# Kernel tuning notes

Hardware: AMD Instinct MI355X
Metric: run time of the kernel (lower is better)

## Reference

```python
import jax, jax.numpy as jnp
import numpy as np

N_HEAD = 8
LN_EPS = 1e-5


def _ln(x, g, b):
    m = jnp.mean(x, axis=-1, keepdims=True)
    v = jnp.mean((x - m) ** 2, axis=-1, keepdims=True)
    return (x - m) * jax.lax.rsqrt(v + LN_EPS) * g + b


def setup_inputs() -> dict:
    B, S, IN, D, F, OUT, L = 4, 2048, 3, 512, 2048, 20, 6
    key = jax.random.key(0)
    ks = jax.random.split(key, 22)
    sc = 0.02
    return {
        'src': jax.random.normal(ks[0], (B, S, IN), jnp.float32),
        'W_in': jax.random.normal(ks[1], (IN, D), jnp.float32) * sc,
        'b_in': jnp.zeros((D,), jnp.float32),
        'Wq': jax.random.normal(ks[2], (L, D, D), jnp.float32) * sc,
        'bq': jnp.zeros((L, D), jnp.float32),
        'Wk': jax.random.normal(ks[3], (L, D, D), jnp.float32) * sc,
        'bk': jnp.zeros((L, D), jnp.float32),
        'Wv': jax.random.normal(ks[4], (L, D, D), jnp.float32) * sc,
        'bv': jnp.zeros((L, D), jnp.float32),
        'Wo': jax.random.normal(ks[5], (L, D, D), jnp.float32) * sc,
        'bo': jnp.zeros((L, D), jnp.float32),
        'ln1_g': jnp.ones((L, D), jnp.float32),
        'ln1_b': jnp.zeros((L, D), jnp.float32),
        'W1': jax.random.normal(ks[6], (L, D, F), jnp.float32) * sc,
        'b1': jnp.zeros((L, F), jnp.float32),
        'W2': jax.random.normal(ks[7], (L, F, D), jnp.float32) * sc,
        'b2': jnp.zeros((L, D), jnp.float32),
        'ln2_g': jnp.ones((L, D), jnp.float32),
        'ln2_b': jnp.zeros((L, D), jnp.float32),
        'W_out': jax.random.normal(ks[8], (D, OUT), jnp.float32) * sc,
        'b_out': jnp.zeros((OUT,), jnp.float32),
    }


def reference(src, W_in, b_in, Wq, bq, Wk, bk, Wv, bv, Wo, bo, ln1_g, ln1_b,
              W1, b1, W2, b2, ln2_g, ln2_b, W_out, b_out):
    x = src @ W_in + b_in            # [B, S, D]
    B, S, D = x.shape
    dh = D // N_HEAD
    scale = 1.0 / np.sqrt(dh).astype(np.float32)

    def layer(x, p):
        wq, biq, wk, bik, wv, biv, wo, bio, g1, be1, w1, bi1, w2, bi2, g2, be2 = p
        q = (x @ wq + biq).reshape(B, S, N_HEAD, dh)
        k = (x @ wk + bik).reshape(B, S, N_HEAD, dh)
        v = (x @ wv + biv).reshape(B, S, N_HEAD, dh)
        # flex_attention with score_mod=None == plain scaled dot-product attention
        scores = jnp.einsum('bqhd,bkhd->bhqk', q, k) * scale
        a = jax.nn.softmax(scores, axis=-1)
        o = jnp.einsum('bhqk,bkhd->bqhd', a, v).reshape(B, S, D)
        attn = o @ wo + bio
        h = _ln(x + attn, g1, be1)                       # post-norm (norm_first=False)
        ff = jax.nn.relu(h @ w1 + bi1) @ w2 + bi2
        h = _ln(h + ff, g2, be2)
        return h, None

    x, _ = jax.lax.scan(layer, x, (Wq, bq, Wk, bk, Wv, bv, Wo, bo,
                                   ln1_g, ln1_b, W1, b1, W2, b2, ln2_g, ln2_b))
    return x @ W_out + b_out         # [B, S, OUT]
```

## Files before the change

### kernel.cpp

```cpp
#include <hip/hip_runtime.h>

typedef unsigned short u16;
typedef unsigned int u32;
typedef __bf16 bf16x8 __attribute__((ext_vector_type(8)));
typedef float f32x4 __attribute__((ext_vector_type(4)));
typedef float f32x16 __attribute__((ext_vector_type(16)));

__device__ __forceinline__ u16 f2bf(float f) {
    union { float f; u32 u; } v; v.f = f;
    u32 r = v.u + 0x7FFFu + ((v.u >> 16) & 1u);
    return (u16)(r >> 16);
}

__device__ __forceinline__ u16 bfu(float x) {
    __bf16 b = (__bf16)x;
    union { __bf16 b; u16 u; } c; c.b = b; return c.u;
}

__device__ __forceinline__ void pl32swap(u32& a, u32& b) {
    asm volatile("v_permlane32_swap_b32 %0, %1" : "+v"(a), "+v"(b));
}

__device__ __forceinline__ void gload16(const u16* g, u16* l) {
    __builtin_amdgcn_global_load_lds((const __attribute__((address_space(1))) void*)g,
                                     (__attribute__((address_space(3))) void*)l, 16, 0, 0);
}

__global__ void wtrans(const float* __restrict__ W, u16* __restrict__ Wt,
                       int K, int N, int rowOff, int dstLd, long long dstStride)
{
    __shared__ float tile[32][33];
    const int l = blockIdx.z;
    const float* Wl = W + (size_t)l * K * N;
    u16* Wtl = Wt + (size_t)l * dstStride;
    const int tx = threadIdx.x, ty = threadIdx.y;
    const int x = blockIdx.x * 32 + tx;
    const int y0 = blockIdx.y * 32;
#pragma unroll
    for (int j = 0; j < 32; j += 8) tile[ty + j][tx] = Wl[(size_t)(y0 + ty + j) * N + x];
    __syncthreads();
    const int n0 = blockIdx.x * 32;
    const int k = y0 + tx;
#pragma unroll
    for (int j = 0; j < 32; j += 8)
        Wtl[(size_t)(rowOff + n0 + ty + j) * dstLd + k] = f2bf(tile[tx][ty + j]);
}

__global__ __launch_bounds__(256) void input_proj(const float* __restrict__ src,
    const float* __restrict__ Wi, const float* __restrict__ bi,
    float* __restrict__ xf, u16* __restrict__ xb)
{
    int idx = blockIdx.x * 256 + threadIdx.x;
    int m = idx >> 9, n = idx & 511;
    float v = bi[n] + src[m * 3] * Wi[n] + src[m * 3 + 1] * Wi[512 + n] + src[m * 3 + 2] * Wi[1024 + n];
    xf[idx] = v;
    xb[idx] = f2bf(v);
}

template<int EPI>
__global__ __launch_bounds__(256) void gemm_bt(
    const u16* __restrict__ A, const u16* __restrict__ Bt,
    const float* __restrict__ bias,
    float* __restrict__ Cf, u16* __restrict__ Cb,
    u16* __restrict__ Qo, u16* __restrict__ Ko, u16* __restrict__ Vo,
    const float* __restrict__ bq, const float* __restrict__ bk, const float* __restrict__ bv,
    int M, int N, int K)
{
    __shared__ u16 As[128 * 64];
    __shared__ u16 Bs[128 * 64];
    const int tid = threadIdx.x;
    const int lane = tid & 63, wid = tid >> 6;
    const int row0 = blockIdx.y * 128, col0 = blockIdx.x * 128;
    const int wr = (wid >> 1) * 64, wc = (wid & 1) * 64;
    const int cc = lane & 15, qg = lane >> 4;
    const int sr = tid >> 3, sg = tid & 7;
    f32x4 acc[4][4] = {};
    for (int k0 = 0; k0 < K; k0 += 64) {
        __syncthreads();
#pragma unroll
        for (int j = 0; j < 4; j++) {
            int r = j * 32 + sr;
            int gsw = (sg ^ (r & 7)) * 8;
            gload16(A + (size_t)(row0 + r) * K + k0 + gsw, &As[(j * 256 + tid) * 8]);
        }
#pragma unroll
        for (int j = 0; j < 4; j++) {
            int r = j * 32 + sr;
            int gsw = (sg ^ (r & 7)) * 8;
            gload16(Bt + (size_t)(col0 + r) * K + k0 + gsw, &Bs[(j * 256 + tid) * 8]);
        }
        __syncthreads();
        bf16x8 af[4][2], bfr[4][2];
#pragma unroll
        for (int i = 0; i < 4; i++) {
            int r = wr + i * 16 + cc;
#pragma unroll
            for (int kk = 0; kk < 2; kk++)
                af[i][kk] = *(const bf16x8*)&As[r * 64 + ((kk * 4 + qg) ^ (r & 7)) * 8];
        }
#pragma unroll
        for (int i = 0; i < 4; i++) {
            int r = wc + i * 16 + cc;
#pragma unroll
            for (int kk = 0; kk < 2; kk++)
                bfr[i][kk] = *(const bf16x8*)&Bs[r * 64 + ((kk * 4 + qg) ^ (r & 7)) * 8];
        }
#pragma unroll
        for (int mi = 0; mi < 4; mi++)
#pragma unroll
            for (int ni = 0; ni < 4; ni++) {
                acc[mi][ni] = __builtin_amdgcn_mfma_f32_16x16x32_bf16(af[mi][0], bfr[ni][0], acc[mi][ni], 0, 0, 0);
                acc[mi][ni] = __builtin_amdgcn_mfma_f32_16x16x32_bf16(af[mi][1], bfr[ni][1], acc[mi][ni], 0, 0, 0);
            }
    }
    const int q4 = qg * 4;
    if (EPI == 2) {
#pragma unroll
        for (int mi = 0; mi < 4; mi++) {
            int grow = row0 + wr + mi * 16 + q4;
            int btok = grow >> 11, srem = grow & 2047;
#pragma unroll
            for (int ni = 0; ni < 4; ni++) {
                int gcol = col0 + wc + ni * 16 + cc;
                int sec = gcol >> 9, f = gcol & 511;
                int hh = f >> 6, dd = f & 63;
                if (sec == 0) {
                    float bb = bq[f];
                    size_t base = (((size_t)btok * 8 + hh) * 2048 + srem) * 64 + dd;
#pragma unroll
                    for (int i = 0; i < 4; i++) Qo[base + (size_t)i * 64] = f2bf((acc[mi][ni][i] + bb) * 0.18033688f);
                } else if (sec == 1) {
                    float bb = bk[f];
                    size_t base = (((size_t)btok * 8 + hh) * 2048 + srem) * 64 + dd;
#pragma unroll
                    for (int i = 0; i < 4; i++) Ko[base + (size_t)i * 64] = f2bf(acc[mi][ni][i] + bb);
                } else {
                    float bb = bv[f];
                    size_t base = (((size_t)btok * 8 + hh) * 64 + dd) * 2048 + srem;
#pragma unroll
                    for (int i = 0; i < 4; i++) Vo[base + i] = f2bf(acc[mi][ni][i] + bb);
                }
            }
        }
    } else {
#pragma unroll
        for (int mi = 0; mi < 4; mi++) {
            int grow = row0 + wr + mi * 16 + q4;
#pragma unroll
            for (int ni = 0; ni < 4; ni++) {
                int gcol = col0 + wc + ni * 16 + cc;
                float bb = bias[gcol];
#pragma unroll
                for (int i = 0; i < 4; i++) {
                    float v = acc[mi][ni][i] + bb;
                    if (EPI == 0) Cf[(size_t)(grow + i) * N + gcol] = v;
                    else          Cb[(size_t)(grow + i) * N + gcol] = f2bf(v > 0.f ? v : 0.f);
                }
            }
        }
    }
}

__global__ __launch_bounds__(256) void gemm_bt_n64(
    const u16* __restrict__ A, const u16* __restrict__ Bt,
    const float* __restrict__ bias, float* __restrict__ Cf,
    int M, int N, int K)
{
    __shared__ u16 As[128 * 64];
    __shared__ u16 Bs[64 * 64];
    const int tid = threadIdx.x;
    const int lane = tid & 63, wid = tid >> 6;
    const int row0 = blockIdx.y * 128, col0 = blockIdx.x * 64;
    const int wr = (wid >> 1) * 64, wc = (wid & 1) * 32;
    const int cc = lane & 15, qg = lane >> 4;
    f32x4 acc[4][2] = {};
    for (int k0 = 0; k0 < K; k0 += 64) {
        __syncthreads();
#pragma unroll
        for (int j = 0; j < 4; j++) {
            int s = j * 256 + tid;
            int r = s >> 3, g = s & 7;
            gload16(A + (size_t)(row0 + r) * K + k0 + (g ^ (r & 7)) * 8, &As[s * 8]);
        }
#pragma unroll
        for (int j = 0; j < 2; j++) {
            int s = j * 256 + tid;
            int r = s >> 3, g = s & 7;
            gload16(Bt + (size_t)(col0 + r) * K + k0 + (g ^ (r & 7)) * 8, &Bs[s * 8]);
        }
        __syncthreads();
        bf16x8 af[4][2], bfr[2][2];
#pragma unroll
        for (int i = 0; i < 4; i++) {
            int r = wr + i * 16 + cc;
#pragma unroll
            for (int kk = 0; kk < 2; kk++) {
                int g = kk * 4 + qg;
                af[i][kk] = *(const bf16x8*)&As[r * 64 + (g ^ (r & 7)) * 8];
            }
        }
#pragma unroll
        for (int i = 0; i < 2; i++) {
            int r = wc + i * 16 + cc;
#pragma unroll
            for (int kk = 0; kk < 2; kk++) {
                int g = kk * 4 + qg;
                bfr[i][kk] = *(const bf16x8*)&Bs[r * 64 + (g ^ (r & 7)) * 8];
            }
        }
#pragma unroll
        for (int mi = 0; mi < 4; mi++)
#pragma unroll
            for (int ni = 0; ni < 2; ni++) {
                acc[mi][ni] = __builtin_amdgcn_mfma_f32_16x16x32_bf16(af[mi][0], bfr[ni][0], acc[mi][ni], 0, 0, 0);
                acc[mi][ni] = __builtin_amdgcn_mfma_f32_16x16x32_bf16(af[mi][1], bfr[ni][1], acc[mi][ni], 0, 0, 0);
            }
    }
    const int q4 = qg * 4;
#pragma unroll
    for (int mi = 0; mi < 4; mi++) {
        int grow = row0 + wr + mi * 16 + q4;
#pragma unroll
        for (int ni = 0; ni < 2; ni++) {
            int gcol = col0 + wc + ni * 16 + cc;
            float bb = bias[gcol];
#pragma unroll
            for (int i = 0; i < 4; i++)
                Cf[(size_t)(grow + i) * N + gcol] = acc[mi][ni][i] + bb;
        }
    }
}

__global__ __launch_bounds__(256) void flash_attn(
    const u16* __restrict__ Qb, const u16* __restrict__ Kb, const u16* __restrict__ Vt,
    u16* __restrict__ Ob)
{
    __shared__ u16 Ks[2][4096];
    __shared__ u16 Vs[2][4096];
    const int tid = threadIdx.x, lane = tid & 63, w = tid >> 6;
    const int l31 = lane & 31, h = lane >> 5;
    const int bh = blockIdx.x, qt = blockIdx.y;
    const u16* Kg = Kb + (size_t)bh * (2048 * 64);
    const u16* Vg = Vt + (size_t)bh * (64 * 2048);

    bf16x8 qf[4];
    {
        const u16* Qrow = Qb + ((size_t)bh * 2048 + (size_t)qt * 128 + w * 32 + l31) * 64;
#pragma unroll
        for (int f = 0; f < 4; f++) qf[f] = *(const bf16x8*)(Qrow + f * 16 + h * 8);
    }
    f32x16 os0{}, os1{};
    float lsum = 0.f;

    const int r8 = lane >> 3;
    const int cswz = ((lane & 7) ^ r8) * 8;
#pragma unroll
    for (int cc = 0; cc < 2; cc++) {
        int c = w * 2 + cc;
        gload16(Kg + (size_t)(c * 8 + r8) * 64 + cswz, &Ks[0][c * 512]);
        gload16(Vg + (size_t)(c * 8 + r8) * 2048 + cswz, &Vs[0][c * 512]);
    }
    const int swz = (l31 & 7) << 3;

    for (int kt = 0; kt < 32; kt++) {
        const int cur = kt & 1;
        asm volatile("s_waitcnt vmcnt(0)" ::: "memory");
        __syncthreads();
        if (kt < 31) {
#pragma unroll
            for (int cc = 0; cc < 2; cc++) {
                int c = w * 2 + cc;
                gload16(Kg + (size_t)(kt + 1) * 4096 + (size_t)(c * 8 + r8) * 64 + cswz, &Ks[cur ^ 1][c * 512]);
                gload16(Vg + (size_t)(c * 8 + r8) * 2048 + (size_t)(kt + 1) * 64 + cswz, &Vs[cur ^ 1][c * 512]);
            }
        }
        f32x16 p0{}, p1{};
        {
            const u16* kb = &Ks[cur][0];
            __builtin_amdgcn_s_setprio(1);
#pragma unroll
            for (int f = 0; f < 4; f++) {
                int colu = (f * 16 + h * 8) ^ swz;
                bf16x8 ka0 = *(const bf16x8*)(kb + l31 * 64 + colu);
                bf16x8 ka1 = *(const bf16x8*)(kb + (32 + l31) * 64 + colu);
                p0 = __builtin_amdgcn_mfma_f32_32x32x16_bf16(ka0, qf[f], p0, 0, 0, 0);
                p1 = __builtin_amdgcn_mfma_f32_32x32x16_bf16(ka1, qf[f], p1, 0, 0, 0);
            }
            __builtin_amdgcn_s_setprio(0);
        }
        float ss[4] = {};
#pragma unroll
        for (int r = 0; r < 16; r++) { float e = __builtin_amdgcn_exp2f(p0[r]); p0[r] = e; ss[r & 3] += e; }
#pragma unroll
        for (int r = 0; r < 16; r++) { float e = __builtin_amdgcn_exp2f(p1[r]); p1[r] = e; ss[r & 3] += e; }
        lsum += (ss[0] + ss[1]) + (ss[2] + ss[3]);
        const u16* vb = &Vs[cur][0];
#pragma unroll
        for (int t = 0; t < 2; t++) {
            u32 pk[8];
#pragma unroll
            for (int j = 0; j < 8; j++) {
                float a = t ? p1[2 * j] : p0[2 * j];
                float b = t ? p1[2 * j + 1] : p0[2 * j + 1];
                pk[j] = (u32)bfu(a) | ((u32)bfu(b) << 16);
            }
            u32 x0 = pk[0], y0 = pk[2]; pl32swap(x0, y0);
            u32 x1 = pk[1], y1 = pk[3]; pl32swap(x1, y1);
            u32 x2 = pk[4], y2 = pk[6]; pl32swap(x2, y2);
            u32 x3 = pk[5], y3 = pk[7]; pl32swap(x3, y3);
            union { u32 u[4]; bf16x8 v; } fA, fB;
            fA.u[0] = x0; fA.u[1] = x1; fA.u[2] = y0; fA.u[3] = y1;
            fB.u[0] = x2; fB.u[1] = x3; fB.u[2] = y2; fB.u[3] = y3;
            __builtin_amdgcn_s_setprio(1);
#pragma unroll
            for (int f = 0; f < 2; f++) {
                bf16x8 pa = f ? fB.v : fA.v;
                int colu = (t * 32 + f * 16 + h * 8) ^ swz;
                bf16x8 v0 = *(const bf16x8*)(vb + l31 * 64 + colu);
                bf16x8 v1 = *(const bf16x8*)(vb + (32 + l31) * 64 + colu);
                os0 = __builtin_amdgcn_mfma_f32_32x32x16_bf16(pa, v0, os0, 0, 0, 0);
                os1 = __builtin_amdgcn_mfma_f32_32x32x16_bf16(pa, v1, os1, 0, 0, 0);
            }
            __builtin_amdgcn_s_setprio(0);
        }
    }
    lsum += __shfl_xor(lsum, 32);
    float rl = 1.f / lsum;
    const int hatt = bh & 7, b_ = bh >> 3;
#pragma unroll
    for (int r = 0; r < 16; r++) {
        int qrow = (r & 3) + 8 * (r >> 2) + 4 * h;
        float rlq = __shfl(rl, qrow);
        int tok = qt * 128 + w * 32 + qrow;
        u16* po = Ob + ((size_t)b_ * 2048 + tok) * 512 + hatt * 64;
        po[l31] = bfu(os0[r] * rlq);
        po[32 + l31] = bfu(os1[r] * rlq);
    }
}

__global__ __launch_bounds__(256) void ln_res(
    const float* __restrict__ X, const float* __restrict__ Y,
    const float* __restrict__ g, const float* __restrict__ bta,
    float* __restrict__ Of, u16* __restrict__ Ob)
{
    const int lane = threadIdx.x & 63;
    const int row = blockIdx.x * 4 + (threadIdx.x >> 6);
    const size_t base = (size_t)row * 512 + lane * 8;
    float4 x0 = *(const float4*)(X + base);
    float4 x1 = *(const float4*)(X + base + 4);
    float4 y0 = *(const float4*)(Y + base);
    float4 y1 = *(const float4*)(Y + base + 4);
    float t[8] = {x0.x + y0.x, x0.y + y0.y, x0.z + y0.z, x0.w + y0.w,
                  x1.x + y1.x, x1.y + y1.y, x1.z + y1.z, x1.w + y1.w};
    float s = 0.f, s2 = 0.f;
#pragma unroll
    for (int j = 0; j < 8; j++) { s += t[j]; s2 += t[j] * t[j]; }
#pragma unroll
    for (int off = 1; off < 64; off <<= 1) { s += __shfl_xor(s, off); s2 += __shfl_xor(s2, off); }
    float mean = s * (1.f / 512.f);
    float var = s2 * (1.f / 512.f) - mean * mean;
    float rs = rsqrtf(var + 1e-5f);
    float4 g0 = *(const float4*)(g + lane * 8);
    float4 g1 = *(const float4*)(g + lane * 8 + 4);
    float4 b0 = *(const float4*)(bta + lane * 8);
    float4 b1 = *(const float4*)(bta + lane * 8 + 4);
    float gg[8] = {g0.x, g0.y, g0.z, g0.w, g1.x, g1.y, g1.z, g1.w};
    float bb[8] = {b0.x, b0.y, b0.z, b0.w, b1.x, b1.y, b1.z, b1.w};
    float o[8];
#pragma unroll
    for (int j = 0; j < 8; j++) o[j] = (t[j] - mean) * rs * gg[j] + bb[j];
    *(float4*)(Of + base) = make_float4(o[0], o[1], o[2], o[3]);
    *(float4*)(Of + base + 4) = make_float4(o[4], o[5], o[6], o[7]);
    u32 p0 = (u32)f2bf(o[0]) | ((u32)f2bf(o[1]) << 16);
    u32 p1 = (u32)f2bf(o[2]) | ((u32)f2bf(o[3]) << 16);
    u32 p2 = (u32)f2bf(o[4]) | ((u32)f2bf(o[5]) << 16);
    u32 p3 = (u32)f2bf(o[6]) | ((u32)f2bf(o[7]) << 16);
    *(uint4*)(Ob + base) = make_uint4(p0, p1, p2, p3);
}

__global__ __launch_bounds__(320) void out_proj(const float* __restrict__ x,
    const float* __restrict__ W, const float* __restrict__ b, float* __restrict__ out)
{
    int t = blockIdx.x * 320 + threadIdx.x;
    int m = t / 20, o = t - m * 20;
    const float* xr = x + (size_t)m * 512;
    float acc = b[o];
#pragma unroll 8
    for (int k = 0; k < 512; k++) acc = fmaf(xr[k], W[k * 20 + o], acc);
    out[(size_t)m * 20 + o] = acc;
}

extern "C" void kernel_launch(void* const* d_in, const int* in_sizes, int n_in,
                              void* d_out, int out_size, void* d_ws, size_t ws_size,
                              hipStream_t stream)
{
    const float* src  = (const float*)d_in[0];
    const float* W_in = (const float*)d_in[1];
    const float* b_in = (const float*)d_in[2];
    const float* Wq   = (const float*)d_in[3];
    const float* bq   = (const float*)d_in[4];
    const float* Wk   = (const float*)d_in[5];
    const float* bk   = (const float*)d_in[6];
    const float* Wv   = (const float*)d_in[7];
    const float* bv   = (const float*)d_in[8];
    const float* Wo   = (const float*)d_in[9];
    const float* bo   = (const float*)d_in[10];
    const float* ln1g = (const float*)d_in[11];
    const float* ln1b = (const float*)d_in[12];
    const float* W1   = (const float*)d_in[13];
    const float* b1   = (const float*)d_in[14];
    const float* W2   = (const float*)d_in[15];
    const float* b2   = (const float*)d_in[16];
    const float* ln2g = (const float*)d_in[17];
    const float* ln2b = (const float*)d_in[18];
    const float* Wout = (const float*)d_in[19];
    const float* bout = (const float*)d_in[20];

    char* ws = (char*)d_ws;
    size_t off = 0;
    auto take = [&](size_t bytes) -> void* {
        off = (off + 255) & ~(size_t)255;
        void* p = ws + off;
        off += bytes;
        return p;
    };
    const size_t TOK = 8192, D = 512;
    u16*   qkvt = (u16*)take(6ull * 1536 * 512 * 2);
    u16*   wot  = (u16*)take(6ull * 512 * 512 * 2);
    u16*   w1t  = (u16*)take(6ull * 2048 * 512 * 2);
    u16*   w2t  = (u16*)take(6ull * 512 * 2048 * 2);
    float* xf   = (float*)take(TOK * D * 4);
    u16*   xb   = (u16*)take(TOK * D * 2);
    u16*   sh4  = (u16*)take(4ull * TOK * D * 2);
    float* scr  = (float*)take(TOK * D * 4);
    float* h1f  = (float*)take(TOK * D * 4);
    u16*   h1b  = (u16*)take(TOK * D * 2);
    if (off > ws_size) return;

    u16* qb  = sh4;
    u16* kb_ = sh4 + TOK * D;
    u16* vtb = sh4 + 2 * TOK * D;
    u16* ob  = sh4 + 3 * TOK * D;
    u16* ffb = sh4;

    dim3 tb(32, 8);
    wtrans<<<dim3(16, 16, 6), tb, 0, stream>>>(Wq, qkvt, 512, 512, 0,    512, 1536ll * 512);
    wtrans<<<dim3(16, 16, 6), tb, 0, stream>>>(Wk, qkvt, 512, 512, 512,  512, 1536ll * 512);
    wtrans<<<dim3(16, 16, 6), tb, 0, stream>>>(Wv, qkvt, 512, 512, 1024, 512, 1536ll * 512);
    wtrans<<<dim3(16, 16, 6), tb, 0, stream>>>(Wo, wot,  512, 512, 0,    512, 512ll * 512);
    wtrans<<<dim3(64, 16, 6), tb, 0, stream>>>(W1, w1t,  512, 2048, 0,   512, 2048ll * 512);
    wtrans<<<dim3(16, 64, 6), tb, 0, stream>>>(W2, w2t,  2048, 512, 0,  2048, 512ll * 2048);

    input_proj<<<16384, 256, 0, stream>>>(src, W_in, b_in, xf, xb);

    for (int l = 0; l < 6; l++) {
        const u16* qkvt_l = qkvt + (size_t)l * 1536 * 512;
        const u16* wot_l  = wot  + (size_t)l * 512 * 512;
        const u16* w1t_l  = w1t  + (size_t)l * 2048 * 512;
        const u16* w2t_l  = w2t  + (size_t)l * 512 * 2048;

        gemm_bt<2><<<dim3(12, 64), 256, 0, stream>>>(xb, qkvt_l, nullptr,
            nullptr, nullptr, qb, kb_, vtb,
            bq + l * 512, bk + l * 512, bv + l * 512, 8192, 1536, 512);

        flash_attn<<<dim3(32, 16), 256, 0, stream>>>(qb, kb_, vtb, ob);

        gemm_bt_n64<<<dim3(8, 64), 256, 0, stream>>>(ob, wot_l, bo + l * 512,
            scr, 8192, 512, 512);

        ln_res<<<2048, 256, 0, stream>>>(xf, scr, ln1g + l * 512, ln1b + l * 512, h1f, h1b);

        gemm_bt<1><<<dim3(16, 64), 256, 0, stream>>>(h1b, w1t_l, b1 + l * 2048,
            nullptr, ffb, nullptr, nullptr, nullptr, nullptr, nullptr, nullptr,
            8192, 2048, 512);

        gemm_bt_n64<<<dim3(8, 64), 256, 0, stream>>>(ffb, w2t_l, b2 + l * 512,
            scr, 8192, 512, 2048);

        ln_res<<<2048, 256, 0, stream>>>(h1f, scr, ln2g + l * 512, ln2b + l * 512, xf, xb);
    }

    out_proj<<<512, 320, 0, stream>>>(xf, Wout, bout, (float*)d_out);
}
```

Measured before the change: 1.106 ms.

## Double-buffer N=512 GEMMs with smaller 64x64 tiles and split out_proj accumulators

The N=512 GEMMs (attention output projection and FFN down-projection) now use 64x64 tiles instead of 128x64, which doubles the grid to 1024 blocks for better CU fill. They also double-buffer LDS so the next K-tile's global loads are issued before the current tile's MFMAs, and they raise wave priority around the MFMA block. The aim is to hide load latency and fix low occupancy and wave count on a 256-CU part, at the cost of less data reuse per block. The final out_proj uses four independent accumulators to break its FMA dependency chain.

Result: no change. 1.106 ms (-0.1%).

```diff
diff --git a/kernel.cpp b/kernel.cpp
--- a/kernel.cpp
+++ b/kernel.cpp
@@ -161,64 +161,67 @@
     }
 }
 
-__global__ __launch_bounds__(256) void gemm_bt_n64(
+__global__ __launch_bounds__(256) void gemm64_db(
     const u16* __restrict__ A, const u16* __restrict__ Bt,
     const float* __restrict__ bias, float* __restrict__ Cf,
     int M, int N, int K)
 {
-    __shared__ u16 As[128 * 64];
-    __shared__ u16 Bs[64 * 64];
+    __shared__ u16 As[2][64 * 64];
+    __shared__ u16 Bs[2][64 * 64];
     const int tid = threadIdx.x;
     const int lane = tid & 63, wid = tid >> 6;
-    const int row0 = blockIdx.y * 128, col0 = blockIdx.x * 64;
-    const int wr = (wid >> 1) * 64, wc = (wid & 1) * 32;
+    const int row0 = blockIdx.y * 64, col0 = blockIdx.x * 64;
+    const int wr = (wid >> 1) * 32, wc = (wid & 1) * 32;
     const int cc = lane & 15, qg = lane >> 4;
-    f32x4 acc[4][2] = {};
+    const int r0 = tid >> 3, g8 = (tid & 7);
+    const int gsw0 = (g8 ^ (r0 & 7)) * 8;
+    const int r1 = r0 + 32;
+    const int gsw1 = (g8 ^ (r1 & 7)) * 8;
+    f32x4 acc[2][2] = {};
+    gload16(A + (size_t)(row0 + r0) * K + gsw0, &As[0][tid * 8]);
+    gload16(A + (size_t)(row0 + r1) * K + gsw1, &As[0][(tid + 256) * 8]);
+    gload16(Bt + (size_t)(col0 + r0) * K + gsw0, &Bs[0][tid * 8]);
+    gload16(Bt + (size_t)(col0 + r1) * K + gsw1, &Bs[0][(tid + 256) * 8]);
+    int cur = 0;
     for (int k0 = 0; k0 < K; k0 += 64) {
+        asm volatile("s_waitcnt vmcnt(0)" ::: "memory");
         __syncthreads();
-#pragma unroll
-        for (int j = 0; j < 4; j++) {
-            int s = j * 256 + tid;
-            int r = s >> 3, g = s & 7;
-            gload16(A + (size_t)(row0 + r) * K + k0 + (g ^ (r & 7)) * 8, &As[s * 8]);
-        }
-#pragma unroll
-        for (int j = 0; j < 2; j++) {
-            int s = j * 256 + tid;
-            int r = s >> 3, g = s & 7;
-            gload16(Bt + (size_t)(col0 + r) * K + k0 + (g ^ (r & 7)) * 8, &Bs[s * 8]);
-        }
-        __syncthreads();
-        bf16x8 af[4][2], bfr[2][2];
-#pragma unroll
-        for (int i = 0; i < 4; i++) {
+        if (k0 + 64 < K) {
+            int kn = k0 + 64, nb = cur ^ 1;
+            gload16(A + (size_t)(row0 + r0) * K + kn + gsw0, &As[nb][tid * 8]);
+            gload16(A + (size_t)(row0 + r1) * K + kn + gsw1, &As[nb][(tid + 256) * 8]);
+            gload16(Bt + (size_t)(col0 + r0) * K + kn + gsw0, &Bs[nb][tid * 8]);
+            gload16(Bt + (size_t)(col0 + r1) * K + kn + gsw1, &Bs[nb][(tid + 256) * 8]);
+        }
+        bf16x8 af[2][2], bfr[2][2];
+#pragma unroll
+        for (int i = 0; i < 2; i++) {
             int r = wr + i * 16 + cc;
 #pragma unroll
-            for (int kk = 0; kk < 2; kk++) {
-                int g = kk * 4 + qg;
-                af[i][kk] = *(const bf16x8*)&As[r * 64 + (g ^ (r & 7)) * 8];
-            }
+            for (int kk = 0; kk < 2; kk++)
+                af[i][kk] = *(const bf16x8*)&As[cur][r * 64 + ((kk * 4 + qg) ^ (r & 7)) * 8];
         }
 #pragma unroll
         for (int i = 0; i < 2; i++) {
             int r = wc + i * 16 + cc;
 #pragma unroll
-            for (int kk = 0; kk < 2; kk++) {
-                int g = kk * 4 + qg;
-                bfr[i][kk] = *(const bf16x8*)&Bs[r * 64 + (g ^ (r & 7)) * 8];
-            }
-        }
-#pragma unroll
-        for (int mi = 0; mi < 4; mi++)
+            for (int kk = 0; kk < 2; kk++)
+                bfr[i][kk] = *(const bf16x8*)&Bs[cur][r * 64 + ((kk * 4 + qg) ^ (r & 7)) * 8];
+        }
+        __builtin_amdgcn_s_setprio(1);
+#pragma unroll
+        for (int mi = 0; mi < 2; mi++)
 #pragma unroll
             for (int ni = 0; ni < 2; ni++) {
                 acc[mi][ni] = __builtin_amdgcn_mfma_f32_16x16x32_bf16(af[mi][0], bfr[ni][0], acc[mi][ni], 0, 0, 0);
                 acc[mi][ni] = __builtin_amdgcn_mfma_f32_16x16x32_bf16(af[mi][1], bfr[ni][1], acc[mi][ni], 0, 0, 0);
             }
+        __builtin_amdgcn_s_setprio(0);
+        cur ^= 1;
     }
     const int q4 = qg * 4;
 #pragma unroll
-    for (int mi = 0; mi < 4; mi++) {
+    for (int mi = 0; mi < 2; mi++) {
         int grow = row0 + wr + mi * 16 + q4;
 #pragma unroll
         for (int ni = 0; ni < 2; ni++) {
@@ -384,10 +387,15 @@
     int t = blockIdx.x * 320 + threadIdx.x;
     int m = t / 20, o = t - m * 20;
     const float* xr = x + (size_t)m * 512;
-    float acc = b[o];
-#pragma unroll 8
-    for (int k = 0; k < 512; k++) acc = fmaf(xr[k], W[k * 20 + o], acc);
-    out[(size_t)m * 20 + o] = acc;
+    float a0 = b[o], a1 = 0.f, a2 = 0.f, a3 = 0.f;
+#pragma unroll 4
+    for (int k = 0; k < 512; k += 4) {
+        a0 = fmaf(xr[k],     W[k * 20 + o],       a0);
+        a1 = fmaf(xr[k + 1], W[(k + 1) * 20 + o], a1);
+        a2 = fmaf(xr[k + 2], W[(k + 2) * 20 + o], a2);
+        a3 = fmaf(xr[k + 3], W[(k + 3) * 20 + o], a3);
+    }
+    out[(size_t)m * 20 + o] = (a0 + a1) + (a2 + a3);
 }
 
 extern "C" void kernel_launch(void* const* d_in, const int* in_sizes, int n_in,
@@ -465,7 +473,7 @@
 
         flash_attn<<<dim3(32, 16), 256, 0, stream>>>(qb, kb_, vtb, ob);
 
-        gemm_bt_n64<<<dim3(8, 64), 256, 0, stream>>>(ob, wot_l, bo + l * 512,
+        gemm64_db<<<dim3(8, 128), 256, 0, stream>>>(ob, wot_l, bo + l * 512,
             scr, 8192, 512, 512);
 
         ln_res<<<2048, 256, 0, stream>>>(xf, scr, ln1g + l * 512, ln1b + l * 512, h1f, h1b);
@@ -474,7 +482,7 @@
             nullptr, ffb, nullptr, nullptr, nullptr, nullptr, nullptr, nullptr,
             8192, 2048, 512);
 
-        gemm_bt_n64<<<dim3(8, 64), 256, 0, stream>>>(ffb, w2t_l, b2 + l * 512,
+        gemm64_db<<<dim3(8, 128), 256, 0, stream>>>(ffb, w2t_l, b2 + l * 512,
             scr, 8192, 512, 2048);
 
         ln_res<<<2048, 256, 0, stream>>>(h1f, scr, ln2g + l * 512, ln2b + l * 512, xf, xb);
```
